# Performance work log

Measured on AMD Instinct MI355X. Metric: run time of the kernel, lower is better.

## Reference

```python
import jax, jax.numpy as jnp
import numpy as np

H = 20  # GRU hidden size (fixed in the module)


def gru_cell(x, h, Wih, Whh, bih, bhh):
    # PyTorch GRU cell math. x: (B, F), h: (B, H)
    gi = x @ Wih.T + bih  # (B, 3H)
    gh = h @ Whh.T + bhh  # (B, 3H)
    i_r, i_z, i_n = jnp.split(gi, 3, axis=-1)
    h_r, h_z, h_n = jnp.split(gh, 3, axis=-1)
    r = jax.nn.sigmoid(i_r + h_r)
    z = jax.nn.sigmoid(i_z + h_z)
    n = jnp.tanh(i_n + r * h_n)
    return (1.0 - z) * n + z * h


def setup_inputs() -> dict:
    key = jax.random.key(0)
    ks = jax.random.split(key, 16)
    B, S, R = 1024, 1024, 12
    F = R + 4 + 4 + 8 + 8  # 36 = input_record_width + embedding output_dim
    x = jax.random.normal(ks[0], (B, S, R), dtype=jnp.float32)
    onehots = jax.random.randint(ks[1], (B, S, 4), 0, 10, dtype=jnp.int64)
    s = 0.1
    inp = {
        'x': x, 'onehots': onehots,
        'emb0': jax.random.normal(ks[2], (10, 4), jnp.float32) * s,
        'emb1': jax.random.normal(ks[3], (20, 4), jnp.float32) * s,
        'emb2': jax.random.normal(ks[4], (50, 8), jnp.float32) * s,
        'emb3': jax.random.normal(ks[5], (100, 8), jnp.float32) * s,
        'Wih1': jax.random.normal(ks[6], (3 * H, F), jnp.float32) * s,
        'Whh1': jax.random.normal(ks[7], (3 * H, H), jnp.float32) * s,
        'bih1': jax.random.normal(ks[8], (3 * H,), jnp.float32) * s,
        'bhh1': jax.random.normal(ks[9], (3 * H,), jnp.float32) * s,
        'Wih2': jax.random.normal(ks[10], (3 * H, F), jnp.float32) * s,
        'Whh2': jax.random.normal(ks[11], (3 * H, H), jnp.float32) * s,
        'bih2': jax.random.normal(ks[12], (3 * H,), jnp.float32) * s,
        'bhh2': jax.random.normal(ks[13], (3 * H,), jnp.float32) * s,
        'Wfc': jax.random.normal(ks[14], (F, H), jnp.float32) * s,
        'bfc': jax.random.normal(ks[15], (F,), jnp.float32) * s,
    }
    return inp


def reference(x, onehots, emb0, emb1, emb2, emb3,
              Wih1, Whh1, bih1, bhh1, Wih2, Whh2, bih2, bhh2, Wfc, bfc):
    # Onehot embedding: lookup per categorical column, concat
    emb = jnp.concatenate([
        emb0[onehots[..., 0]], emb1[onehots[..., 1]],
        emb2[onehots[..., 2]], emb3[onehots[..., 3]],
    ], axis=-1)
    xin = jnp.concatenate([x, emb], axis=-1)  # (B, S, F)
    origin = xin
    B, S, F = xin.shape

    # Encoder GRU (gru1) over the sequence; keep only final hidden state
    h0 = jnp.zeros((B, H), xin.dtype)

    def enc_step(h, xt):
        return gru_cell(xt, h, Wih1, Whh1, bih1, bhh1), None

    h_last, _ = jax.lax.scan(enc_step, h0, jnp.swapaxes(xin, 0, 1))
    h = jnp.tanh(h_last)
    x0 = jnp.tanh(h @ Wfc.T + bfc)  # first decoded step

    def dec_step(carry, _):
        xprev, hprev = carry
        hnew = jnp.tanh(gru_cell(xprev, hprev, Wih2, Whh2, bih2, bhh2))
        xnew = jnp.tanh(hnew @ Wfc.T + bfc)
        return (xnew, hnew), xnew

    _, rest = jax.lax.scan(dec_step, (x0, h), None, length=S - 1)  # (S-1, B, F)
    xs = jnp.concatenate([x0[None], rest], axis=0)  # (S, B, F)
    xs = jnp.swapaxes(xs, 0, 1)[:, ::-1]  # (B, S, F), flipped along time
    return (origin, xs)
```

## Files before the change

### kernel.cpp

```cpp
#include <hip/hip_runtime.h>

#define BATCH 1024
#define SEQ   1024
#define FDIM  36
#define HID   20
#define G3    60
#define GIPAD 60
#define NROWS (BATCH*SEQ)

typedef float v2f __attribute__((ext_vector_type(2)));

__device__ __forceinline__ float fast_sigmoid(float x){
    return __builtin_amdgcn_rcpf(1.0f + __expf(-x));
}
__device__ __forceinline__ float fast_tanh(float x){
    return fmaf(-2.0f, __builtin_amdgcn_rcpf(1.0f + __expf(2.0f*x)), 1.0f);
}

#define READLANE_F(v, u) __int_as_float(__builtin_amdgcn_readlane(__float_as_int(v), (u)))

template<bool WRITE_GI>
__global__ __launch_bounds__(256, 1)
void prep_kernel(const float* __restrict__ x,
                 const int* __restrict__ oh,
                 const float* __restrict__ e0, const float* __restrict__ e1,
                 const float* __restrict__ e2, const float* __restrict__ e3,
                 const float* __restrict__ Wih1g, const float* __restrict__ bih1g,
                 float* __restrict__ origin, float* __restrict__ gibuf)
{
    const int lane  = threadIdx.x & 63;
    const int wslot = threadIdx.x >> 6;
    const int w = blockIdx.x * 4 + wslot;
    const int ROWS = 64;
    const int r0 = w * ROWS;

    const int j = lane;
    const float* tbl; int ohc, eshift, sub;
    if (j < 16)      { tbl = e0; ohc = 0; eshift = 2; sub = j - 12; }
    else if (j < 20) { tbl = e1; ohc = 1; eshift = 2; sub = j - 16; }
    else if (j < 28) { tbl = e2; ohc = 2; eshift = 3; sub = j - 20; }
    else             { tbl = e3; ohc = 3; eshift = 3; sub = j - 28; }
    if (sub < 0) sub = 0;
    if (sub > 7) sub = 7;
    const bool from_x = (j < 12);
    const float* pa = from_x ? (x + j) : (tbl + sub);

    float w1[FDIM]; float bi = 0.f;
    const int k = lane < G3 ? lane : G3 - 1;
    if (WRITE_GI) {
        #pragma unroll
        for (int jj = 0; jj < FDIM; jj++) w1[jj] = Wih1g[k * FDIM + jj];
        bi = bih1g[k];
    }

    int   ohq[8];
    float valq[8];
    #pragma unroll
    for (int s = 0; s < 8; s++) {
        int r = r0 + s; if (r >= NROWS) r = NROWS - 1;
        ohq[s] = oh[r * 4 + ohc];
    }
    #pragma unroll
    for (int s = 0; s < 8; s++) {
        int r = r0 + s; if (r >= NROWS) r = NROWS - 1;
        int off = from_x ? (r * 12) : (ohq[s] << eshift);
        valq[s] = pa[off];
        int r2 = r0 + s + 8; if (r2 >= NROWS) r2 = NROWS - 1;
        ohq[s] = oh[r2 * 4 + ohc];
    }

    for (int i = 0; i < ROWS; i++) {
        const int s = i & 7;
        const float val = valq[s];
        int rv = r0 + i + 8;  if (rv >= NROWS) rv = NROWS - 1;
        int off = from_x ? (rv * 12) : (ohq[s] << eshift);
        valq[s] = pa[off];
        int ro = r0 + i + 16; if (ro >= NROWS) ro = NROWS - 1;
        ohq[s] = oh[ro * 4 + ohc];

        const int row = r0 + i;
        if (lane < FDIM) origin[row * FDIM + lane] = val;
        if (WRITE_GI) {
            float a0 = bi, a1 = 0.f, a2 = 0.f, a3 = 0.f;
            #pragma unroll
            for (int jj = 0; jj < FDIM; jj += 4) {
                a0 = fmaf(w1[jj + 0], READLANE_F(val, jj + 0), a0);
                a1 = fmaf(w1[jj + 1], READLANE_F(val, jj + 1), a1);
                a2 = fmaf(w1[jj + 2], READLANE_F(val, jj + 2), a2);
                a3 = fmaf(w1[jj + 3], READLANE_F(val, jj + 3), a3);
            }
            if (lane < G3) gibuf[row * GIPAD + lane] = (a0 + a1) + (a2 + a3);
        }
    }
}

template<bool USE_GI>
__global__ __launch_bounds__(256, 1)
void gru_kernel(const float* __restrict__ xin,
                const float* __restrict__ gibuf,
                const float* __restrict__ Wih1g, const float* __restrict__ Whh1g,
                const float* __restrict__ bih1g, const float* __restrict__ bhh1g,
                const float* __restrict__ Wih2g, const float* __restrict__ Whh2g,
                const float* __restrict__ bih2g, const float* __restrict__ bhh2g,
                const float* __restrict__ Wfcg,  const float* __restrict__ bfcg,
                float* __restrict__ out2)
{
    __shared__ __align__(16) float xsh[4][64];
    const int lane  = threadIdx.x & 63;
    const int wslot = threadIdx.x >> 6;
    const int b = __builtin_amdgcn_readfirstlane(blockIdx.x * 4 + wslot);

    const int k  = lane < G3   ? lane : G3 - 1;
    const int kf = lane < FDIM ? lane : FDIM - 1;

    float whh1[HID], whh2[HID], wfc[HID];
    v2f wih2p[FDIM/2];
    #pragma unroll
    for (int u = 0; u < HID; u++) whh1[u] = Whh1g[k * HID + u];
    #pragma unroll
    for (int q = 0; q < FDIM/2; q++) wih2p[q] = ((const v2f*)(Wih2g + k * FDIM))[q];
    #pragma unroll
    for (int u = 0; u < HID; u++) whh2[u] = Whh2g[k * HID + u];
    #pragma unroll
    for (int u = 0; u < HID; u++) wfc[u] = Wfcg[kf * HID + u];
    const float bh1 = bhh1g[k];
    const float bi2 = bih2g[k], bh2 = bhh2g[k];
    const float bf  = bfcg[kf];

    float hs[HID];
    #pragma unroll
    for (int u = 0; u < HID; u++) hs[u] = 0.0f;
    float hv = 0.0f;

    if (USE_GI) {
        const float* gb = gibuf + (size_t)b * SEQ * GIPAD + k;
        float gq[8];
        #pragma unroll
        for (int u = 0; u < 8; u++) gq[u] = gb[(size_t)u * GIPAD];
        for (int t = 0; t < SEQ; t += 8) {
            #pragma unroll
            for (int u = 0; u < 8; u++) {
                float giv = gq[u];
                int nr = t + u + 8; nr = nr < SEQ ? nr : SEQ - 1;
                gq[u] = gb[(size_t)nr * GIPAD];
                float h0 = bh1, h1 = 0.f, h2 = 0.f, h3 = 0.f;
                #pragma unroll
                for (int uu = 0; uu < HID; uu += 4) {
                    h0 = fmaf(whh1[uu + 0], hs[uu + 0], h0);
                    h1 = fmaf(whh1[uu + 1], hs[uu + 1], h1);
                    h2 = fmaf(whh1[uu + 2], hs[uu + 2], h2);
                    h3 = fmaf(whh1[uu + 3], hs[uu + 3], h3);
                }
                float gh = (h0 + h1) + (h2 + h3);
                float v   = giv + gh;
                float vz  = __shfl(v,   (lane + 20) & 63);
                float in_ = __shfl(giv, (lane + 40) & 63);
                float hn  = __shfl(gh,  (lane + 40) & 63);
                float r = fast_sigmoid(v);
                float z = fast_sigmoid(vz);
                float n = fast_tanh(fmaf(r, hn, in_));
                hv = n + z * (hv - n);
                #pragma unroll
                for (int uu = 0; uu < HID; uu++) hs[uu] = READLANE_F(hv, uu);
            }
        }
    } else {
        float wih1[FDIM]; float bi1;
        #pragma unroll
        for (int jj = 0; jj < FDIM; jj++) wih1[jj] = Wih1g[k * FDIM + jj];
        bi1 = bih1g[k];
        const float* xbase = xin + (size_t)b * SEQ * FDIM;
        float xa[FDIM], xb[FDIM];
        #pragma unroll
        for (int jj = 0; jj < FDIM; jj++) xa[jj] = xbase[jj];
#define ENC_STEP(XS) do {                                                    \
        float g0 = bi1, g1 = 0.f, g2 = 0.f, g3 = 0.f;                        \
        _Pragma("unroll")                                                    \
        for (int jj = 0; jj < FDIM; jj += 4) {                               \
            g0 = fmaf(wih1[jj + 0], XS[jj + 0], g0);                         \
            g1 = fmaf(wih1[jj + 1], XS[jj + 1], g1);                         \
            g2 = fmaf(wih1[jj + 2], XS[jj + 2], g2);                         \
            g3 = fmaf(wih1[jj + 3], XS[jj + 3], g3);                         \
        }                                                                    \
        float gi = (g0 + g1) + (g2 + g3);                                    \
        float h0 = bh1, h1 = 0.f, h2 = 0.f, h3 = 0.f;                        \
        _Pragma("unroll")                                                    \
        for (int uu = 0; uu < HID; uu += 4) {                                \
            h0 = fmaf(whh1[uu + 0], hs[uu + 0], h0);                         \
            h1 = fmaf(whh1[uu + 1], hs[uu + 1], h1);                         \
            h2 = fmaf(whh1[uu + 2], hs[uu + 2], h2);                         \
            h3 = fmaf(whh1[uu + 3], hs[uu + 3], h3);                         \
        }                                                                    \
        float gh = (h0 + h1) + (h2 + h3);                                    \
        float v   = gi + gh;                                                 \
        float vz  = __shfl(v,  (lane + 20) & 63);                            \
        float in_ = __shfl(gi, (lane + 40) & 63);                            \
        float hn  = __shfl(gh, (lane + 40) & 63);                            \
        float r = fast_sigmoid(v);                                           \
        float z = fast_sigmoid(vz);                                          \
        float n = fast_tanh(fmaf(r, hn, in_));                               \
        hv = n + z * (hv - n);                                               \
        _Pragma("unroll")                                                    \
        for (int uu = 0; uu < HID; uu++) hs[uu] = READLANE_F(hv, uu);        \
    } while (0)
        for (int t = 0; t < SEQ; t += 2) {
            const float* p1 = xbase + (size_t)(t + 1) * FDIM;
            #pragma unroll
            for (int jj = 0; jj < FDIM; jj++) xb[jj] = p1[jj];
            ENC_STEP(xa);
            const float* p2 = xbase + (size_t)(t + 2) * FDIM;
            #pragma unroll
            for (int jj = 0; jj < FDIM; jj++) xa[jj] = p2[jj];
            ENC_STEP(xb);
        }
    }

    float hvd = fast_tanh(hv);
    #pragma unroll
    for (int u = 0; u < HID; u++) hs[u] = READLANE_F(hvd, u);

    float* orow = out2 + ((size_t)b * SEQ + (SEQ - 1)) * FDIM;

    float xv;
    {
        float a0 = bf, a1 = 0.f, a2 = 0.f, a3 = 0.f;
        #pragma unroll
        for (int u = 0; u < HID; u += 4) {
            a0 = fmaf(wfc[u + 0], hs[u + 0], a0);
            a1 = fmaf(wfc[u + 1], hs[u + 1], a1);
            a2 = fmaf(wfc[u + 2], hs[u + 2], a2);
            a3 = fmaf(wfc[u + 3], hs[u + 3], a3);
        }
        xv = fast_tanh((a0 + a1) + (a2 + a3));
    }
    if (lane < FDIM) orow[lane] = xv;
    xsh[wslot][lane] = xv;

    const v2f* xp = (const v2f*)xsh[wslot];
    for (int d = 1; d < SEQ; ++d) {
        orow -= FDIM;
        v2f xs2[FDIM/2];
        #pragma unroll
        for (int q = 0; q < FDIM/2; q++) xs2[q] = xp[q];
        float h0 = bh2, h1 = 0.f, h2 = 0.f, h3 = 0.f;
        #pragma unroll
        for (int u = 0; u < HID; u += 4) {
            h0 = fmaf(whh2[u + 0], hs[u + 0], h0);
            h1 = fmaf(whh2[u + 1], hs[u + 1], h1);
            h2 = fmaf(whh2[u + 2], hs[u + 2], h2);
            h3 = fmaf(whh2[u + 3], hs[u + 3], h3);
        }
        float gh = (h0 + h1) + (h2 + h3);
        v2f accA = {bi2, 0.f}, accB = {0.f, 0.f};
        #pragma unroll
        for (int q = 0; q < FDIM/2; q += 2) {
            accA = __builtin_elementwise_fma(wih2p[q],     xs2[q],     accA);
            accB = __builtin_elementwise_fma(wih2p[q + 1], xs2[q + 1], accB);
        }
        float gi = (accA.x + accB.x) + (accA.y + accB.y);
        float v   = gi + gh;
        float vz  = __shfl(v,  (lane + 20) & 63);
        float in_ = __shfl(gi, (lane + 40) & 63);
        float hn  = __shfl(gh, (lane + 40) & 63);
        float r = fast_sigmoid(v);
        float z = fast_sigmoid(vz);
        float n = fast_tanh(fmaf(r, hn, in_));
        float hraw = n + z * (hvd - n);
        hvd = fast_tanh(hraw);
        #pragma unroll
        for (int u = 0; u < HID; u++) hs[u] = READLANE_F(hvd, u);
        float a0 = bf, a1 = 0.f, a2 = 0.f, a3 = 0.f;
        #pragma unroll
        for (int u = 0; u < HID; u += 4) {
            a0 = fmaf(wfc[u + 0], hs[u + 0], a0);
            a1 = fmaf(wfc[u + 1], hs[u + 1], a1);
            a2 = fmaf(wfc[u + 2], hs[u + 2], a2);
            a3 = fmaf(wfc[u + 3], hs[u + 3], a3);
        }
        xv = fast_tanh((a0 + a1) + (a2 + a3));
        if (lane < FDIM) orow[lane] = xv;
        xsh[wslot][lane] = xv;
    }
}

extern "C" void kernel_launch(void* const* d_in, const int* in_sizes, int n_in,
                              void* d_out, int out_size, void* d_ws, size_t ws_size,
                              hipStream_t stream) {
    const float* x    = (const float*)d_in[0];
    const int*   oh   = (const int*)d_in[1];
    const float* e0   = (const float*)d_in[2];
    const float* e1   = (const float*)d_in[3];
    const float* e2   = (const float*)d_in[4];
    const float* e3   = (const float*)d_in[5];
    const float* Wih1 = (const float*)d_in[6];
    const float* Whh1 = (const float*)d_in[7];
    const float* bih1 = (const float*)d_in[8];
    const float* bhh1 = (const float*)d_in[9];
    const float* Wih2 = (const float*)d_in[10];
    const float* Whh2 = (const float*)d_in[11];
    const float* bih2 = (const float*)d_in[12];
    const float* bhh2 = (const float*)d_in[13];
    const float* Wfc  = (const float*)d_in[14];
    const float* bfc  = (const float*)d_in[15];

    float* out    = (float*)d_out;
    float* origin = out;
    float* out2   = out + (size_t)BATCH * SEQ * FDIM;
    float* gibuf  = (float*)d_ws;

    const size_t gi_bytes = (size_t)BATCH * SEQ * GIPAD * sizeof(float);
    const int prep_blocks = NROWS / (4 * 64);

    if (ws_size >= gi_bytes) {
        prep_kernel<true><<<prep_blocks, 256, 0, stream>>>(x, oh, e0, e1, e2, e3,
                                                           Wih1, bih1, origin, gibuf);
        gru_kernel<true><<<(BATCH * 64) / 256, 256, 0, stream>>>(origin, gibuf,
            Wih1, Whh1, bih1, bhh1, Wih2, Whh2, bih2, bhh2, Wfc, bfc, out2);
    } else {
        prep_kernel<false><<<prep_blocks, 256, 0, stream>>>(x, oh, e0, e1, e2, e3,
                                                            Wih1, bih1, origin, gibuf);
        gru_kernel<false><<<(BATCH * 64) / 256, 256, 0, stream>>>(origin, gibuf,
            Wih1, Whh1, bih1, bhh1, Wih2, Whh2, bih2, bhh2, Wfc, bfc, out2);
    }
}
```

Measured before the change: 1.077 ms.

## Shrink prep rows per wave, use LDS broadcast and packed FMA for input projection

The prep kernel now handles 16 rows per wave instead of 64, which launches four times as many blocks, and its launch bounds now allow 4 blocks per CU. The pipelined prefetch queue is replaced by batched loads issued up front. The input-projection dot product now broadcasts each row through shared memory as float4 reads and uses packed v2f FMAs instead of 36 readlanes. The GRU recurrence loop drops the clamped prefetch index by splitting off the last chunk, and the non-workspace path is simplified to one step per iteration. The aim is more memory-level parallelism and fewer scalar broadcast instructions in prep, at the cost of LDS traffic and a wave-local store/load through shared memory without an explicit barrier.

```diff
diff --git a/kernel.cpp b/kernel.cpp
--- a/kernel.cpp
+++ b/kernel.cpp
@@ -7,6 +7,7 @@
 #define G3    60
 #define GIPAD 60
 #define NROWS (BATCH*SEQ)
+#define PROWS 16
 
 typedef float v2f __attribute__((ext_vector_type(2)));
 
@@ -20,7 +21,7 @@
 #define READLANE_F(v, u) __int_as_float(__builtin_amdgcn_readlane(__float_as_int(v), (u)))
 
 template<bool WRITE_GI>
-__global__ __launch_bounds__(256, 1)
+__global__ __launch_bounds__(256, 4)
 void prep_kernel(const float* __restrict__ x,
                  const int* __restrict__ oh,
                  const float* __restrict__ e0, const float* __restrict__ e1,
@@ -28,11 +29,11 @@
                  const float* __restrict__ Wih1g, const float* __restrict__ bih1g,
                  float* __restrict__ origin, float* __restrict__ gibuf)
 {
+    __shared__ __align__(16) float xsh[4][64];
     const int lane  = threadIdx.x & 63;
     const int wslot = threadIdx.x >> 6;
     const int w = blockIdx.x * 4 + wslot;
-    const int ROWS = 64;
-    const int r0 = w * ROWS;
+    const int r0 = w * PROWS;
 
     const int j = lane;
     const float* tbl; int ohc, eshift, sub;
@@ -45,51 +46,41 @@
     const bool from_x = (j < 12);
     const float* pa = from_x ? (x + j) : (tbl + sub);
 
-    float w1[FDIM]; float bi = 0.f;
-    const int k = lane < G3 ? lane : G3 - 1;
+    v2f w1p[FDIM/2]; float bi = 0.f;
     if (WRITE_GI) {
-        #pragma unroll
-        for (int jj = 0; jj < FDIM; jj++) w1[jj] = Wih1g[k * FDIM + jj];
+        const int k = lane < G3 ? lane : G3 - 1;
+        #pragma unroll
+        for (int q = 0; q < FDIM/2; q++) w1p[q] = ((const v2f*)(Wih1g + k * FDIM))[q];
         bi = bih1g[k];
     }
 
-    int   ohq[8];
-    float valq[8];
-    #pragma unroll
-    for (int s = 0; s < 8; s++) {
-        int r = r0 + s; if (r >= NROWS) r = NROWS - 1;
-        ohq[s] = oh[r * 4 + ohc];
-    }
-    #pragma unroll
-    for (int s = 0; s < 8; s++) {
-        int r = r0 + s; if (r >= NROWS) r = NROWS - 1;
-        int off = from_x ? (r * 12) : (ohq[s] << eshift);
-        valq[s] = pa[off];
-        int r2 = r0 + s + 8; if (r2 >= NROWS) r2 = NROWS - 1;
-        ohq[s] = oh[r2 * 4 + ohc];
-    }
-
-    for (int i = 0; i < ROWS; i++) {
-        const int s = i & 7;
-        const float val = valq[s];
-        int rv = r0 + i + 8;  if (rv >= NROWS) rv = NROWS - 1;
-        int off = from_x ? (rv * 12) : (ohq[s] << eshift);
-        valq[s] = pa[off];
-        int ro = r0 + i + 16; if (ro >= NROWS) ro = NROWS - 1;
-        ohq[s] = oh[ro * 4 + ohc];
-
-        const int row = r0 + i;
-        if (lane < FDIM) origin[row * FDIM + lane] = val;
+    int ohv[PROWS];
+    #pragma unroll
+    for (int s = 0; s < PROWS; s++) ohv[s] = oh[(r0 + s) * 4 + ohc];
+    float valv[PROWS];
+    #pragma unroll
+    for (int s = 0; s < PROWS; s++) {
+        int off = from_x ? ((r0 + s) * 12) : (ohv[s] << eshift);
+        valv[s] = pa[off];
+    }
+
+    const float4* xp4 = (const float4*)xsh[wslot];
+    #pragma unroll
+    for (int s = 0; s < PROWS; s++) {
+        const int row = r0 + s;
+        if (lane < FDIM) origin[row * FDIM + lane] = valv[s];
         if (WRITE_GI) {
-            float a0 = bi, a1 = 0.f, a2 = 0.f, a3 = 0.f;
+            xsh[wslot][lane] = valv[s];
+            v2f a0 = {bi, 0.f}, a1 = {0.f, 0.f};
             #pragma unroll
-            for (int jj = 0; jj < FDIM; jj += 4) {
-                a0 = fmaf(w1[jj + 0], READLANE_F(val, jj + 0), a0);
-                a1 = fmaf(w1[jj + 1], READLANE_F(val, jj + 1), a1);
-                a2 = fmaf(w1[jj + 2], READLANE_F(val, jj + 2), a2);
-                a3 = fmaf(w1[jj + 3], READLANE_F(val, jj + 3), a3);
+            for (int q = 0; q < 9; q++) {
+                float4 xv4 = xp4[q];
+                v2f xlo = {xv4.x, xv4.y}, xhi = {xv4.z, xv4.w};
+                a0 = __builtin_elementwise_fma(w1p[2*q],     xlo, a0);
+                a1 = __builtin_elementwise_fma(w1p[2*q + 1], xhi, a1);
             }
-            if (lane < G3) gibuf[row * GIPAD + lane] = (a0 + a1) + (a2 + a3);
+            float g = (a0.x + a1.x) + (a0.y + a1.y);
+            if (lane < G3) gibuf[row * GIPAD + lane] = g;
         }
     }
 }
@@ -132,58 +123,8 @@
     for (int u = 0; u < HID; u++) hs[u] = 0.0f;
     float hv = 0.0f;
 
-    if (USE_GI) {
-        const float* gb = gibuf + (size_t)b * SEQ * GIPAD + k;
-        float gq[8];
-        #pragma unroll
-        for (int u = 0; u < 8; u++) gq[u] = gb[(size_t)u * GIPAD];
-        for (int t = 0; t < SEQ; t += 8) {
-            #pragma unroll
-            for (int u = 0; u < 8; u++) {
-                float giv = gq[u];
-                int nr = t + u + 8; nr = nr < SEQ ? nr : SEQ - 1;
-                gq[u] = gb[(size_t)nr * GIPAD];
-                float h0 = bh1, h1 = 0.f, h2 = 0.f, h3 = 0.f;
-                #pragma unroll
-                for (int uu = 0; uu < HID; uu += 4) {
-                    h0 = fmaf(whh1[uu + 0], hs[uu + 0], h0);
-                    h1 = fmaf(whh1[uu + 1], hs[uu + 1], h1);
-                    h2 = fmaf(whh1[uu + 2], hs[uu + 2], h2);
-                    h3 = fmaf(whh1[uu + 3], hs[uu + 3], h3);
-                }
-                float gh = (h0 + h1) + (h2 + h3);
-                float v   = giv + gh;
-                float vz  = __shfl(v,   (lane + 20) & 63);
-                float in_ = __shfl(giv, (lane + 40) & 63);
-                float hn  = __shfl(gh,  (lane + 40) & 63);
-                float r = fast_sigmoid(v);
-                float z = fast_sigmoid(vz);
-                float n = fast_tanh(fmaf(r, hn, in_));
-                hv = n + z * (hv - n);
-                #pragma unroll
-                for (int uu = 0; uu < HID; uu++) hs[uu] = READLANE_F(hv, uu);
-            }
-        }
-    } else {
-        float wih1[FDIM]; float bi1;
-        #pragma unroll
-        for (int jj = 0; jj < FDIM; jj++) wih1[jj] = Wih1g[k * FDIM + jj];
-        bi1 = bih1g[k];
-        const float* xbase = xin + (size_t)b * SEQ * FDIM;
-        float xa[FDIM], xb[FDIM];
-        #pragma unroll
-        for (int jj = 0; jj < FDIM; jj++) xa[jj] = xbase[jj];
-#define ENC_STEP(XS) do {                                                    \
-        float g0 = bi1, g1 = 0.f, g2 = 0.f, g3 = 0.f;                        \
-        _Pragma("unroll")                                                    \
-        for (int jj = 0; jj < FDIM; jj += 4) {                               \
-            g0 = fmaf(wih1[jj + 0], XS[jj + 0], g0);                         \
-            g1 = fmaf(wih1[jj + 1], XS[jj + 1], g1);                         \
-            g2 = fmaf(wih1[jj + 2], XS[jj + 2], g2);                         \
-            g3 = fmaf(wih1[jj + 3], XS[jj + 3], g3);                         \
-        }                                                                    \
-        float gi = (g0 + g1) + (g2 + g3);                                    \
-        float h0 = bh1, h1 = 0.f, h2 = 0.f, h3 = 0.f;                        \
+#define GATE_STEP(GIV, BH) do {                                              \
+        float h0 = BH, h1 = 0.f, h2 = 0.f, h3 = 0.f;                         \
         _Pragma("unroll")                                                    \
         for (int uu = 0; uu < HID; uu += 4) {                                \
             h0 = fmaf(whh1[uu + 0], hs[uu + 0], h0);                         \
@@ -192,10 +133,10 @@
             h3 = fmaf(whh1[uu + 3], hs[uu + 3], h3);                         \
         }                                                                    \
         float gh = (h0 + h1) + (h2 + h3);                                    \
-        float v   = gi + gh;                                                 \
-        float vz  = __shfl(v,  (lane + 20) & 63);                            \
-        float in_ = __shfl(gi, (lane + 40) & 63);                            \
-        float hn  = __shfl(gh, (lane + 40) & 63);                            \
+        float v   = (GIV) + gh;                                              \
+        float vz  = __shfl(v,    (lane + 20) & 63);                          \
+        float in_ = __shfl((GIV),(lane + 40) & 63);                          \
+        float hn  = __shfl(gh,   (lane + 40) & 63);                          \
         float r = fast_sigmoid(v);                                           \
         float z = fast_sigmoid(vz);                                          \
         float n = fast_tanh(fmaf(r, hn, in_));                               \
@@ -203,15 +144,48 @@
         _Pragma("unroll")                                                    \
         for (int uu = 0; uu < HID; uu++) hs[uu] = READLANE_F(hv, uu);        \
     } while (0)
-        for (int t = 0; t < SEQ; t += 2) {
-            const float* p1 = xbase + (size_t)(t + 1) * FDIM;
+
+    if (USE_GI) {
+        const float* gb = gibuf + (size_t)b * SEQ * GIPAD + k;
+        float gq[8];
+        #pragma unroll
+        for (int u = 0; u < 8; u++) gq[u] = gb[(size_t)u * GIPAD];
+        for (int t = 0; t < SEQ; t += 8) {
+            if (t + 8 < SEQ) {
+                #pragma unroll
+                for (int u = 0; u < 8; u++) {
+                    float giv = gq[u];
+                    gq[u] = gb[(size_t)(t + u + 8) * GIPAD];
+                    GATE_STEP(giv, bh1);
+                }
+            } else {
+                #pragma unroll
+                for (int u = 0; u < 8; u++) {
+                    GATE_STEP(gq[u], bh1);
+                }
+            }
+        }
+    } else {
+        float wih1[FDIM]; float bi1;
+        #pragma unroll
+        for (int jj = 0; jj < FDIM; jj++) wih1[jj] = Wih1g[k * FDIM + jj];
+        bi1 = bih1g[k];
+        const float* xbase = xin + (size_t)b * SEQ * FDIM;
+        float xa[FDIM];
+        for (int t = 0; t < SEQ; t++) {
+            const float* p = xbase + (size_t)t * FDIM;
             #pragma unroll
-            for (int jj = 0; jj < FDIM; jj++) xb[jj] = p1[jj];
-            ENC_STEP(xa);
-            const float* p2 = xbase + (size_t)(t + 2) * FDIM;
+            for (int jj = 0; jj < FDIM; jj++) xa[jj] = p[jj];
+            float g0 = bi1, g1 = 0.f, g2 = 0.f, g3 = 0.f;
             #pragma unroll
-            for (int jj = 0; jj < FDIM; jj++) xa[jj] = p2[jj];
-            ENC_STEP(xb);
+            for (int jj = 0; jj < FDIM; jj += 4) {
+                g0 = fmaf(wih1[jj + 0], xa[jj + 0], g0);
+                g1 = fmaf(wih1[jj + 1], xa[jj + 1], g1);
+                g2 = fmaf(wih1[jj + 2], xa[jj + 2], g2);
+                g3 = fmaf(wih1[jj + 3], xa[jj + 3], g3);
+            }
+            float giv = (g0 + g1) + (g2 + g3);
+            GATE_STEP(giv, bh1);
         }
     }
 
@@ -309,7 +283,7 @@
     float* gibuf  = (float*)d_ws;
 
     const size_t gi_bytes = (size_t)BATCH * SEQ * GIPAD * sizeof(float);
-    const int prep_blocks = NROWS / (4 * 64);
+    const int prep_blocks = NROWS / (4 * PROWS);
 
     if (ws_size >= gi_bytes) {
         prep_kernel<true><<<prep_blocks, 256, 0, stream>>>(x, oh, e0, e1, e2, e3,
```

Measured after the change: 1.020 ms. -5.3%, faster.
